# Optimization experiments

Hardware: AMD Instinct MI355X
Metric: run time of the kernel (lower is better)

Reference implementation:

```python
import jax, jax.numpy as jnp
import numpy as np
import math

D_MODEL = 1024
NUM_HEADS = 16
D_K = D_MODEL // NUM_HEADS
B, L = 2, 2048
ROPE_BASE = 10000.0


def _rope_cos_sin(seq_len, dim, dtype=jnp.float32):
    inv_freq = 1.0 / (ROPE_BASE ** (jnp.arange(0, dim, 2, dtype=jnp.float32) / dim))
    t = jnp.arange(seq_len, dtype=jnp.float32)
    freqs = jnp.outer(t, inv_freq)            # [L, dim/2]
    emb = jnp.concatenate([freqs, freqs], -1)  # [L, dim]
    return jnp.cos(emb).astype(dtype), jnp.sin(emb).astype(dtype)


def _apply_rope(x, cos, sin):
    # x: [B, H, L, d_k]; cos/sin: [L, d_k]
    x1, x2 = jnp.split(x, 2, axis=-1)
    rotated = jnp.concatenate([-x2, x1], axis=-1)
    return x * cos + rotated * sin


def setup_inputs() -> dict:
    key = jax.random.key(0)
    ks = jax.random.split(key, 12)
    s = 1.0 / math.sqrt(D_MODEL)
    inp = {
        "query": jax.random.normal(ks[0], (B, L, D_MODEL), jnp.float32),
        "key":   jax.random.normal(ks[1], (B, L, D_MODEL), jnp.float32),
        "value": jax.random.normal(ks[2], (B, L, D_MODEL), jnp.float32),
        "mask":  jnp.triu(jnp.ones((L, L), jnp.bool_), k=1)[None, None],  # causal, True = masked
        "Wq": jax.random.uniform(ks[3], (D_MODEL, D_MODEL), jnp.float32, -s, s),
        "bq": jnp.zeros((D_MODEL,), jnp.float32),
        "Wk": jax.random.uniform(ks[4], (D_MODEL, D_MODEL), jnp.float32, -s, s),
        "bk": jnp.zeros((D_MODEL,), jnp.float32),
        "Wv": jax.random.uniform(ks[5], (D_MODEL, D_MODEL), jnp.float32, -s, s),
        "bv": jnp.zeros((D_MODEL,), jnp.float32),
        "Wo": jax.random.uniform(ks[6], (D_MODEL, D_MODEL), jnp.float32, -s, s),
        "bo": jnp.zeros((D_MODEL,), jnp.float32),
    }
    return inp


def reference(query, key, value, mask, Wq, bq, Wk, bk, Wv, bv, Wo, bo):
    b, l, _ = query.shape
    def proj(x, W, bias):
        return (x @ W.T + bias).reshape(b, l, NUM_HEADS, D_K).transpose(0, 2, 1, 3)
    q = proj(query, Wq, bq)   # [B, H, L, d_k]
    k = proj(key,   Wk, bk)
    v = proj(value, Wv, bv)
    cos, sin = _rope_cos_sin(l, D_K, q.dtype)
    q = _apply_rope(q, cos, sin)
    k = _apply_rope(k, cos, sin)
    scale = 1.0 / math.sqrt(D_K)
    att = jnp.einsum('bhqd,bhkd->bhqk', q, k) * scale
    att = jnp.where(mask, jnp.finfo(att.dtype).min, att)
    att = jax.nn.softmax(att, axis=-1)
    out = jnp.einsum('bhqk,bhkd->bhqd', att, v)
    out = out.transpose(0, 2, 1, 3).reshape(b, l, D_MODEL)
    return out @ Wo.T + bo
```

## Files before the change

kernel.cpp:

```cpp
#include <hip/hip_runtime.h>
#include <cstdint>

typedef _Float16 half_t;
using half8 = __attribute__((ext_vector_type(8))) half_t;
using half4 = __attribute__((ext_vector_type(4))) half_t;
using f32x4 = __attribute__((ext_vector_type(4))) float;
using f32x16 = __attribute__((ext_vector_type(16))) float;

#define LSEQ 2048
#define DM   1024
#define NH   16
#define DK   64

__device__ inline void gload_lds16(const void* g, void* l) {
    __builtin_amdgcn_global_load_lds(
        (const __attribute__((address_space(1))) uint32_t*)g,
        (__attribute__((address_space(3))) uint32_t*)l, 16, 0, 0);
}

__device__ inline uint32_t pk2(float a, float b) {
    auto h = __builtin_amdgcn_cvt_pkrtz(a, b);
    return __builtin_bit_cast(uint32_t, h);
}

__device__ inline float ex2(float x) { return __builtin_amdgcn_exp2f(x); }

__global__ __launch_bounds__(256) void cvt_kernel(
    const float* __restrict__ q, const float* __restrict__ k, const float* __restrict__ v,
    const float* __restrict__ wq, const float* __restrict__ wk,
    const float* __restrict__ wv, const float* __restrict__ wo,
    half_t* __restrict__ dst)
{
    long tid = (long)blockIdx.x * 256 + threadIdx.x;
    long e = tid * 4;
    const float* src;
    long off;
    if (e < 12582912L) {
        int a = (int)(e >> 22);
        src = (a == 0) ? q : (a == 1) ? k : v;
        off = e & 4194303L;
    } else {
        long ew = e - 12582912L;
        int w = (int)(ew >> 20);
        src = (w == 0) ? wq : (w == 1) ? wk : (w == 2) ? wv : wo;
        off = ew & 1048575L;
    }
    float4 x = *(const float4*)(src + off);
    half4 o;
    o[0] = (half_t)x.x; o[1] = (half_t)x.y; o[2] = (half_t)x.z; o[3] = (half_t)x.w;
    *(half4*)(dst + e) = o;
}

__global__ __launch_bounds__(256) void rope_tab(float* __restrict__ cosT, float* __restrict__ sinT) {
    int tid = blockIdx.x * 256 + threadIdx.x;
    int j = tid >> 11;
    int pos = tid & 2047;
    float invf = powf(10000.0f, -(float)j / 32.0f);
    float a = (float)pos * invf;
    cosT[tid] = cosf(a);
    sinT[tid] = sinf(a);
}

__global__ __launch_bounds__(256, 3) void qkv_gemm(
    const half_t* __restrict__ XH, const half_t* __restrict__ WH,
    const float* __restrict__ bq, const float* __restrict__ bk, const float* __restrict__ bv,
    half_t* __restrict__ QF, half_t* __restrict__ KF, half_t* __restrict__ VF,
    const float* __restrict__ cosT, const float* __restrict__ sinT)
{
    __shared__ alignas(16) unsigned short sA[2][128 * 32];
    __shared__ alignas(16) unsigned short sB[2][128 * 32];
    const int mode = blockIdx.z;
    const half_t* A  = XH + (long)mode * 4194304L;
    const half_t* Bw = WH + (long)mode * 1048576L;
    const float* bias = (mode == 0) ? bq : (mode == 1) ? bk : bv;

    const int tid = threadIdx.x;
    const int lane = tid & 63, wid = tid >> 6;
    const int g = lane >> 4, c = lane & 15;
    const int wr = wid >> 1, wc = wid & 1;
    const int row0 = blockIdx.y * 128, col0 = blockIdx.x * 128;

    f32x4 acc[4][4] = {};
    const int srow = lane >> 2;
    const int scol = ((lane & 3) ^ ((lane >> 3) & 3)) * 8;
    const int kx   = (g ^ ((c >> 1) & 3)) * 8;

    auto stage = [&](int buf, int k0) {
#pragma unroll
        for (int i = 0; i < 2; ++i) {
            int r = wid * 32 + i * 16;
            gload_lds16(A  + (long)(row0 + r + srow) * DM + k0 + scol, &sA[buf][r * 32]);
            gload_lds16(Bw + (long)(col0 + r + srow) * DM + k0 + scol, &sB[buf][r * 32]);
        }
    };

    stage(0, 0);
    __syncthreads();
    int cur = 0;
#pragma unroll 1
    for (int k0 = 0; k0 < DM; k0 += 32) {
        if (k0 + 32 < DM) stage(cur ^ 1, k0 + 32);
        half8 af[4], bf[4];
#pragma unroll
        for (int m = 0; m < 4; ++m)
            af[m] = *(const half8*)&sA[cur][(wr * 64 + m * 16 + c) * 32 + kx];
#pragma unroll
        for (int n = 0; n < 4; ++n)
            bf[n] = *(const half8*)&sB[cur][(wc * 64 + n * 16 + c) * 32 + kx];
#pragma unroll
        for (int m = 0; m < 4; ++m)
#pragma unroll
            for (int n = 0; n < 4; ++n)
                acc[m][n] = __builtin_amdgcn_mfma_f32_16x16x32_f16(af[m], bf[n], acc[m][n], 0, 0, 0);
        __syncthreads();
        cur ^= 1;
    }

    if (mode == 2) {
        const int h = blockIdx.x * 2 + wc;
#pragma unroll
        for (int n = 0; n < 4; ++n) {
            int col = col0 + wc * 64 + n * 16 + c;
            int d = n * 16 + c;
            float bvv = bias[col];
#pragma unroll
            for (int m = 0; m < 4; ++m) {
                int row = row0 + wr * 64 + m * 16 + g * 4;
                int b = row >> 11, pos = row & 2047;
                int bh = b * NH + h;
                long idx = (((((long)bh * 32 + (pos >> 6)) * 2 + (d >> 5)) * 4
                             + ((pos >> 4) & 3)) * 64
                            + (((pos >> 3) & 1) * 32 + (d & 31))) * 8 + (pos & 7);
                half4 o;
#pragma unroll
                for (int r = 0; r < 4; ++r) o[r] = (half_t)(acc[m][n][r] + bvv);
                *(half4*)(VF + idx) = o;
            }
        }
    } else {
        const float SC = (mode == 0) ? 0.125f * 1.44269504f : 1.0f;
        half_t* OF = (mode == 0) ? QF : KF;
#pragma unroll
        for (int np = 0; np < 2; ++np) {
            int col1 = col0 + wc * 64 + np * 16 + c;
            int h = col1 >> 6;
            int d1 = np * 16 + c;
            float b1 = bias[col1], b2 = bias[col1 + 32];
            const float* Cp = cosT + d1 * 2048;
            const float* Sp = sinT + d1 * 2048;
#pragma unroll
            for (int m = 0; m < 4; ++m) {
                int row = row0 + wr * 64 + m * 16 + g * 4;
                int pos0 = row & 2047;
                float4 cv4 = *(const float4*)(Cp + pos0);
                float4 sv4 = *(const float4*)(Sp + pos0);
#pragma unroll
                for (int r = 0; r < 4; ++r) {
                    int pos = pos0 + r;
                    int b = (row + r) >> 11;
                    int bh = b * NH + h;
                    float cv = ((const float*)&cv4)[r];
                    float sv = ((const float*)&sv4)[r];
                    float x1 = acc[m][np][r] + b1;
                    float x2 = acc[m][np + 2][r] + b2;
                    long kbase = ((long)(bh * 64 + (pos >> 5)) * 4) * 512
                               + ((c >> 3) * 32 + (pos & 31)) * 8 + (c & 7);
                    OF[kbase + (long)np * 512]       = (half_t)((x1 * cv - x2 * sv) * SC);
                    OF[kbase + (long)(np + 2) * 512] = (half_t)((x2 * cv + x1 * sv) * SC);
                }
            }
        }
    }
}

__global__ __launch_bounds__(256, 3) void out_gemm(
    const half_t* __restrict__ A, const half_t* __restrict__ Bw,
    const float* __restrict__ bias, float* __restrict__ o32)
{
    __shared__ alignas(16) unsigned short sA[2][128 * 32];
    __shared__ alignas(16) unsigned short sB[2][128 * 32];
    const int tid = threadIdx.x;
    const int lane = tid & 63, wid = tid >> 6;
    const int g = lane >> 4, c = lane & 15;
    const int wr = wid >> 1, wc = wid & 1;
    const int row0 = blockIdx.y * 128, col0 = blockIdx.x * 128;

    f32x4 acc[4][4] = {};
    const int srow = lane >> 2;
    const int scol = ((lane & 3) ^ ((lane >> 3) & 3)) * 8;
    const int kx   = (g ^ ((c >> 1) & 3)) * 8;

    auto stage = [&](int buf, int k0) {
#pragma unroll
        for (int i = 0; i < 2; ++i) {
            int r = wid * 32 + i * 16;
            gload_lds16(A  + (long)(row0 + r + srow) * DM + k0 + scol, &sA[buf][r * 32]);
            gload_lds16(Bw + (long)(col0 + r + srow) * DM + k0 + scol, &sB[buf][r * 32]);
        }
    };

    stage(0, 0);
    __syncthreads();
    int cur = 0;
#pragma unroll 1
    for (int k0 = 0; k0 < DM; k0 += 32) {
        if (k0 + 32 < DM) stage(cur ^ 1, k0 + 32);
        half8 af[4], bf[4];
#pragma unroll
        for (int m = 0; m < 4; ++m)
            af[m] = *(const half8*)&sA[cur][(wr * 64 + m * 16 + c) * 32 + kx];
#pragma unroll
        for (int n = 0; n < 4; ++n)
            bf[n] = *(const half8*)&sB[cur][(wc * 64 + n * 16 + c) * 32 + kx];
#pragma unroll
        for (int m = 0; m < 4; ++m)
#pragma unroll
            for (int n = 0; n < 4; ++n)
                acc[m][n] = __builtin_amdgcn_mfma_f32_16x16x32_f16(af[m], bf[n], acc[m][n], 0, 0, 0);
        __syncthreads();
        cur ^= 1;
    }
#pragma unroll
    for (int n = 0; n < 4; ++n) {
        int col = col0 + wc * 64 + n * 16 + c;
        float bv = bias[col];
#pragma unroll
        for (int m = 0; m < 4; ++m)
#pragma unroll
            for (int r = 0; r < 4; ++r) {
                int row = row0 + wr * 64 + m * 16 + g * 4 + r;
                o32[(long)row * DM + col] = acc[m][n][r] + bv;
            }
    }
}

__global__ __launch_bounds__(512, 2) void attn_k(
    const half_t* __restrict__ QF, const half_t* __restrict__ KF,
    const half_t* __restrict__ VF, half_t* __restrict__ AO)
{
    __shared__ half_t sK[2 * 4096];
    __shared__ half_t sV[2 * 4096];

    const int tid = threadIdx.x;
    const int lane = tid & 63, wid = tid >> 6;
    const int pr = blockIdx.x >> 5;
    const int bh = blockIdx.x & 31;
    const int qc = lane & 31, hi = lane >> 5;
    const int b = bh >> 4, h = bh & 15;
    const int lo8 = lane * 8;
    const int sub = wid & 3, grp = wid >> 2;

    const half_t* QU = QF + (long)bh * 131072;
    const half_t* KU = KF + (long)bh * 131072;
    const half_t* VU = VF + (long)bh * 131072;

    const int t1 = 15 - pr;
    const int t  = grp ? pr : t1;
    const int qb = 128 * t + 32 * sub;
    const int kend = qb + 32;
    const int kmax = 128 * t1 + 128;

    half8 qf[4];
#pragma unroll
    for (int dc = 0; dc < 4; ++dc)
        qf[dc] = *(const half8*)(QU + (qb >> 5) * 2048 + dc * 512 + lo8);

    f32x16 acc[2] = {};
    float lp[16];
#pragma unroll
    for (int r = 0; r < 16; ++r) lp[r] = 0.0f;
    float m = -INFINITY;

    union PB { uint32_t u[4]; half8 h8; };

    auto stage = [&](int buf, int k0) {
        gload_lds16(KU + (long)k0 * 64 + wid * 512 + lo8, sK + buf * 4096 + wid * 512);
        gload_lds16(VU + (long)k0 * 64 + wid * 512 + lo8, sV + buf * 4096 + wid * 512);
    };

    stage(0, 0);
    __syncthreads();

    int cur = 0;
#pragma unroll 1
    for (int k0 = 0; k0 < kmax; k0 += 64) {
        int kn = k0 + 64;
        if (kn < kmax) stage(cur ^ 1, kn);

        if (k0 < kend) {
            const half_t* bK = sK + cur * 4096;
            const half_t* bV = sV + cur * 4096;
            half8 kf0[4], kf1[4], vf[2][4];
#pragma unroll
            for (int dc = 0; dc < 4; ++dc) {
                kf0[dc] = *(const half8*)(bK + dc * 512 + lo8);
                kf1[dc] = *(const half8*)(bK + 2048 + dc * 512 + lo8);
            }
#pragma unroll
            for (int dt = 0; dt < 2; ++dt)
#pragma unroll
                for (int kc = 0; kc < 4; ++kc)
                    vf[dt][kc] = *(const half8*)(bV + (dt * 4 + kc) * 512 + lo8);

            f32x16 s0 = {}, s1 = {};
            __builtin_amdgcn_s_setprio(1);
#pragma unroll
            for (int dc = 0; dc < 4; ++dc) s0 = __builtin_amdgcn_mfma_f32_32x32x16_f16(kf0[dc], qf[dc], s0, 0, 0, 0);
#pragma unroll
            for (int dc = 0; dc < 4; ++dc) s1 = __builtin_amdgcn_mfma_f32_32x32x16_f16(kf1[dc], qf[dc], s1, 0, 0, 0);
            __builtin_amdgcn_s_setprio(0);

            if (kn >= kend) {
                int qg = qb + qc;
#pragma unroll
                for (int r = 0; r < 16; ++r) {
                    int crow = (r & 3) + 8 * (r >> 2) + 4 * hi;
                    if (k0 + crow > qg)      s0[r] = -INFINITY;
                    if (k0 + 32 + crow > qg) s1[r] = -INFINITY;
                }
            }

            float mx[8];
#pragma unroll
            for (int r = 0; r < 8; ++r)
                mx[r] = fmaxf(fmaxf(s0[r], s0[8 + r]), fmaxf(s1[r], s1[8 + r]));
#pragma unroll
            for (int st = 4; st >= 1; st >>= 1)
#pragma unroll
                for (int r = 0; r < 4; ++r)
                    if (r < st) mx[r] = fmaxf(mx[r], mx[r + st]);
            float pm = fmaxf(mx[0], __shfl_xor(mx[0], 32, 64));
            if (__any(pm > m + 8.0f)) {
                float mn = fmaxf(m, pm);
                float sc = ex2(m - mn);
#pragma unroll
                for (int r = 0; r < 16; ++r) {
                    acc[0][r] *= sc; acc[1][r] *= sc; lp[r] *= sc;
                }
                m = mn;
            }
#pragma unroll
            for (int r = 0; r < 16; ++r) {
                s0[r] = ex2(s0[r] - m);
                s1[r] = ex2(s1[r] - m);
                lp[r] += s0[r] + s1[r];
            }

            uint32_t A0[8], A1[8];
#pragma unroll
            for (int i = 0; i < 8; ++i) {
                A0[i] = pk2(s0[2 * i], s0[2 * i + 1]);
                A1[i] = pk2(s1[2 * i], s1[2 * i + 1]);
            }
            PB B00, B01, B10, B11;
            {
                auto r0 = __builtin_amdgcn_permlane32_swap(A0[0], A0[2], false, false);
                B00.u[0] = r0[0]; B00.u[2] = r0[1];
                auto r1 = __builtin_amdgcn_permlane32_swap(A0[1], A0[3], false, false);
                B00.u[1] = r1[0]; B00.u[3] = r1[1];
                auto r2 = __builtin_amdgcn_permlane32_swap(A0[4], A0[6], false, false);
                B01.u[0] = r2[0]; B01.u[2] = r2[1];
                auto r3 = __builtin_amdgcn_permlane32_swap(A0[5], A0[7], false, false);
                B01.u[1] = r3[0]; B01.u[3] = r3[1];
                auto r4 = __builtin_amdgcn_permlane32_swap(A1[0], A1[2], false, false);
                B10.u[0] = r4[0]; B10.u[2] = r4[1];
                auto r5 = __builtin_amdgcn_permlane32_swap(A1[1], A1[3], false, false);
                B10.u[1] = r5[0]; B10.u[3] = r5[1];
                auto r6 = __builtin_amdgcn_permlane32_swap(A1[4], A1[6], false, false);
                B11.u[0] = r6[0]; B11.u[2] = r6[1];
                auto r7 = __builtin_amdgcn_permlane32_swap(A1[5], A1[7], false, false);
                B11.u[1] = r7[0]; B11.u[3] = r7[1];
            }

            __builtin_amdgcn_s_setprio(1);
#pragma unroll
            for (int dt = 0; dt < 2; ++dt) {
                acc[dt] = __builtin_amdgcn_mfma_f32_32x32x16_f16(vf[dt][0], B00.h8, acc[dt], 0, 0, 0);
                acc[dt] = __builtin_amdgcn_mfma_f32_32x32x16_f16(vf[dt][1], B01.h8, acc[dt], 0, 0, 0);
                acc[dt] = __builtin_amdgcn_mfma_f32_32x32x16_f16(vf[dt][2], B10.h8, acc[dt], 0, 0, 0);
                acc[dt] = __builtin_amdgcn_mfma_f32_32x32x16_f16(vf[dt][3], B11.h8, acc[dt], 0, 0, 0);
            }
            __builtin_amdgcn_s_setprio(0);
        }
        __syncthreads();
        cur ^= 1;
    }

    float ls = lp[0];
#pragma unroll
    for (int r = 1; r < 16; ++r) ls += lp[r];
    float l = ls + __shfl_xor(ls, 32, 64);
    float inv = 1.0f / l;
    long obase = ((long)(b * LSEQ + qb + qc)) * DM + h * 64;
#pragma unroll
    for (int dt = 0; dt < 2; ++dt)
#pragma unroll
        for (int rg = 0; rg < 4; ++rg) {
            half4 o;
#pragma unroll
            for (int e = 0; e < 4; ++e) o[e] = (half_t)(acc[dt][4 * rg + e] * inv);
            *(half4*)(AO + obase + dt * 32 + 8 * rg + 4 * hi) = o;
        }
}

extern "C" void kernel_launch(void* const* d_in, const int* in_sizes, int n_in,
                              void* d_out, int out_size, void* d_ws, size_t ws_size,
                              hipStream_t stream) {
    const float* q  = (const float*)d_in[0];
    const float* k  = (const float*)d_in[1];
    const float* v  = (const float*)d_in[2];
    const float* wq = (const float*)d_in[4];
    const float* bq = (const float*)d_in[5];
    const float* wk = (const float*)d_in[6];
    const float* bk = (const float*)d_in[7];
    const float* wv = (const float*)d_in[8];
    const float* bv = (const float*)d_in[9];
    const float* wo = (const float*)d_in[10];
    const float* bo = (const float*)d_in[11];

    uint8_t* wsb = (uint8_t*)d_ws;
    half_t* XH = (half_t*)wsb;
    half_t* WH = XH + 12582912L;
    float*  COS = (float*)(wsb + 33554432L);
    float*  SIN = (float*)(wsb + 33816576L);
    half_t* QF = (half_t*)(wsb + 34078720L);
    half_t* KF = (half_t*)(wsb + 42467328L);
    half_t* VF = (half_t*)(wsb + 50855936L);
    half_t* AO = (half_t*)(wsb + 59244544L);

    cvt_kernel<<<16384, 256, 0, stream>>>(q, k, v, wq, wk, wv, wo, XH);
    rope_tab<<<256, 256, 0, stream>>>(COS, SIN);

    qkv_gemm<<<dim3(8, 32, 3), 256, 0, stream>>>(XH, WH, bq, bk, bv, QF, KF, VF, COS, SIN);

    attn_k<<<256, 512, 0, stream>>>(QF, KF, VF, AO);

    out_gemm<<<dim3(8, 32), 256, 0, stream>>>(AO, WH + 3145728L, bo, (float*)d_out);
}
```

Baseline: 125.7 us.

## Fuse fp32-to-fp16 activation conversion into QKV GEMM A-tile loads

Removes the separate conversion pass over the query/key/value activations. The QKV GEMM now reads fp32 activations directly into registers, packs them to fp16 and writes them to swizzled LDS after the MFMAs for the current tile. This saves a full write and re-read of a 24 MB fp16 copy. In exchange, each GEMM block re-reads A as fp32 from global memory across all 8 column blocks, doubling A traffic per block, and adds register pressure and VALU conversion work inside the loop.

```diff
diff --git a/kernel.cpp b/kernel.cpp
--- a/kernel.cpp
+++ b/kernel.cpp
@@ -25,26 +25,16 @@
 
 __device__ inline float ex2(float x) { return __builtin_amdgcn_exp2f(x); }
 
-__global__ __launch_bounds__(256) void cvt_kernel(
-    const float* __restrict__ q, const float* __restrict__ k, const float* __restrict__ v,
+__global__ __launch_bounds__(256) void cvt_w(
     const float* __restrict__ wq, const float* __restrict__ wk,
     const float* __restrict__ wv, const float* __restrict__ wo,
     half_t* __restrict__ dst)
 {
     long tid = (long)blockIdx.x * 256 + threadIdx.x;
     long e = tid * 4;
-    const float* src;
-    long off;
-    if (e < 12582912L) {
-        int a = (int)(e >> 22);
-        src = (a == 0) ? q : (a == 1) ? k : v;
-        off = e & 4194303L;
-    } else {
-        long ew = e - 12582912L;
-        int w = (int)(ew >> 20);
-        src = (w == 0) ? wq : (w == 1) ? wk : (w == 2) ? wv : wo;
-        off = ew & 1048575L;
-    }
+    int w = (int)(e >> 20);
+    const float* src = (w == 0) ? wq : (w == 1) ? wk : (w == 2) ? wv : wo;
+    long off = e & 1048575L;
     float4 x = *(const float4*)(src + off);
     half4 o;
     o[0] = (half_t)x.x; o[1] = (half_t)x.y; o[2] = (half_t)x.z; o[3] = (half_t)x.w;
@@ -62,7 +52,8 @@
 }
 
 __global__ __launch_bounds__(256, 3) void qkv_gemm(
-    const half_t* __restrict__ XH, const half_t* __restrict__ WH,
+    const float* __restrict__ Aq, const float* __restrict__ Ak, const float* __restrict__ Av,
+    const half_t* __restrict__ WH,
     const float* __restrict__ bq, const float* __restrict__ bk, const float* __restrict__ bv,
     half_t* __restrict__ QF, half_t* __restrict__ KF, half_t* __restrict__ VF,
     const float* __restrict__ cosT, const float* __restrict__ sinT)
@@ -70,7 +61,7 @@
     __shared__ alignas(16) unsigned short sA[2][128 * 32];
     __shared__ alignas(16) unsigned short sB[2][128 * 32];
     const int mode = blockIdx.z;
-    const half_t* A  = XH + (long)mode * 4194304L;
+    const float* A32 = (mode == 0) ? Aq : (mode == 1) ? Ak : Av;
     const half_t* Bw = WH + (long)mode * 1048576L;
     const float* bias = (mode == 0) ? bq : (mode == 1) ? bk : bv;
 
@@ -82,24 +73,51 @@
 
     f32x4 acc[4][4] = {};
     const int srow = lane >> 2;
-    const int scol = ((lane & 3) ^ ((lane >> 3) & 3)) * 8;
+    const int swz  = ((lane & 3) ^ ((lane >> 3) & 3)) * 8;
+    const int ccol = (lane & 3) * 8;
     const int kx   = (g ^ ((c >> 1) & 3)) * 8;
 
-    auto stage = [&](int buf, int k0) {
+    float4 ar[2][2];
+    auto loadA = [&](int k0) {
+#pragma unroll
+        for (int i = 0; i < 2; ++i) {
+            const float* p = A32 + (long)(row0 + wid * 32 + i * 16 + srow) * DM + k0 + ccol;
+            ar[i][0] = *(const float4*)(p);
+            ar[i][1] = *(const float4*)(p + 4);
+        }
+    };
+    auto writeA = [&](int buf) {
+#pragma unroll
+        for (int i = 0; i < 2; ++i) {
+            int r = wid * 32 + i * 16 + srow;
+            union { uint32_t u[4]; half8 h8; } o;
+            o.u[0] = pk2(ar[i][0].x, ar[i][0].y);
+            o.u[1] = pk2(ar[i][0].z, ar[i][0].w);
+            o.u[2] = pk2(ar[i][1].x, ar[i][1].y);
+            o.u[3] = pk2(ar[i][1].z, ar[i][1].w);
+            *(half8*)&sA[buf][r * 32 + swz] = o.h8;
+        }
+    };
+    auto stageB = [&](int buf, int k0) {
 #pragma unroll
         for (int i = 0; i < 2; ++i) {
             int r = wid * 32 + i * 16;
-            gload_lds16(A  + (long)(row0 + r + srow) * DM + k0 + scol, &sA[buf][r * 32]);
-            gload_lds16(Bw + (long)(col0 + r + srow) * DM + k0 + scol, &sB[buf][r * 32]);
+            gload_lds16(Bw + (long)(col0 + r + srow) * DM + k0 + swz, &sB[buf][r * 32]);
         }
     };
 
-    stage(0, 0);
+    loadA(0);
+    stageB(0, 0);
+    writeA(0);
     __syncthreads();
     int cur = 0;
 #pragma unroll 1
     for (int k0 = 0; k0 < DM; k0 += 32) {
-        if (k0 + 32 < DM) stage(cur ^ 1, k0 + 32);
+        const bool hasNext = (k0 + 32 < DM);
+        if (hasNext) {
+            loadA(k0 + 32);
+            stageB(cur ^ 1, k0 + 32);
+        }
         half8 af[4], bf[4];
 #pragma unroll
         for (int m = 0; m < 4; ++m)
@@ -112,6 +130,7 @@
 #pragma unroll
             for (int n = 0; n < 4; ++n)
                 acc[m][n] = __builtin_amdgcn_mfma_f32_16x16x32_f16(af[m], bf[n], acc[m][n], 0, 0, 0);
+        if (hasNext) writeA(cur ^ 1);
         __syncthreads();
         cur ^= 1;
     }
@@ -419,8 +438,7 @@
     const float* bo = (const float*)d_in[11];
 
     uint8_t* wsb = (uint8_t*)d_ws;
-    half_t* XH = (half_t*)wsb;
-    half_t* WH = XH + 12582912L;
+    half_t* WH = (half_t*)wsb;
     float*  COS = (float*)(wsb + 33554432L);
     float*  SIN = (float*)(wsb + 33816576L);
     half_t* QF = (half_t*)(wsb + 34078720L);
@@ -428,10 +446,10 @@
     half_t* VF = (half_t*)(wsb + 50855936L);
     half_t* AO = (half_t*)(wsb + 59244544L);
 
-    cvt_kernel<<<16384, 256, 0, stream>>>(q, k, v, wq, wk, wv, wo, XH);
+    cvt_w<<<4096, 256, 0, stream>>>(wq, wk, wv, wo, WH);
     rope_tab<<<256, 256, 0, stream>>>(COS, SIN);
 
-    qkv_gemm<<<dim3(8, 32, 3), 256, 0, stream>>>(XH, WH, bq, bk, bv, QF, KF, VF, COS, SIN);
+    qkv_gemm<<<dim3(8, 32, 3), 256, 0, stream>>>(q, k, v, WH, bq, bk, bv, QF, KF, VF, COS, SIN);
 
     attn_k<<<256, 512, 0, stream>>>(QF, KF, VF, AO);
 
```

Measured after the change: 145.5 us. 15.8% more time.
